# Optimization experiments

Measured on AMD Instinct MI355X. Metric: run time of the kernel, lower is better.

The kernel has to match this reference:

```python
import jax, jax.numpy as jnp
import numpy as np

B, T, C = 4, 2048, 1024
NH = 16
HS = C // NH


def setup_inputs() -> dict:
    key = jax.random.key(0)
    k1, k2, k3, k4, k5 = jax.random.split(key, 5)
    s_in = 1.0 / np.sqrt(C)
    x = jax.random.normal(k1, (B, T, C), dtype=jnp.float32)
    w_attn = jax.random.normal(k2, (C, 3 * C), dtype=jnp.float32) * s_in
    b_attn = jnp.zeros((3 * C,), dtype=jnp.float32)
    w_proj = jax.random.normal(k3, (C, C), dtype=jnp.float32) * s_in
    b_proj = jnp.zeros((C,), dtype=jnp.float32)
    return {"x": x, "w_attn": w_attn, "b_attn": b_attn,
            "w_proj": w_proj, "b_proj": b_proj}


def reference(x, w_attn, b_attn, w_proj, b_proj):
    Bsz, Tlen, Cdim = x.shape
    qkv = x @ w_attn + b_attn                      # (B,T,3C)
    q, k, v = jnp.split(qkv, 3, axis=2)
    # (B,T,C) -> (B,nh,T,hs)
    def heads(t):
        return t.reshape(Bsz, Tlen, NH, HS).transpose(0, 2, 1, 3)
    q, k, v = heads(q), heads(k), heads(v)
    scale = 1.0 / np.sqrt(HS).astype(np.float32)
    att = jnp.einsum('bhqd,bhkd->bhqk', q, k) * scale  # (B,nh,T,T)
    causal = jnp.tril(jnp.ones((Tlen, Tlen), dtype=bool))
    att = jnp.where(causal, att, -jnp.inf)
    att = jax.nn.softmax(att, axis=-1)
    y = jnp.einsum('bhqk,bhkd->bhqd', att, v)      # (B,nh,T,hs)
    y = y.transpose(0, 2, 1, 3).reshape(Bsz, Tlen, Cdim)
    return y @ w_proj + b_proj
```

## Files before the change

kernel.cpp:

```cpp
#include <hip/hip_runtime.h>
#include <hip/hip_bf16.h>

#define BB 4
#define TT 2048
#define CCH 1024
#define NHH 16
#define HSS 64
#define MROWS (BB * TT)
#define QKV_ELEMS (64 * 2048 * 64)

typedef __attribute__((ext_vector_type(8))) short short8;
typedef __attribute__((ext_vector_type(4))) float f32x4;

#define CVTPK(d, a, b) asm("v_cvt_pk_bf16_f32 %0, %1, %2" : "=v"(d) : "v"(a), "v"(b))

static __device__ __forceinline__ unsigned short bf16_of(float f) {
  union { float f; unsigned u; } v; v.f = f;
  unsigned u = v.u;
  return (unsigned short)((u + 0x7FFFu + ((u >> 16) & 1u)) >> 16);
}

__global__ __launch_bounds__(256) void cast_f32_bf16(const float* __restrict__ in,
                                                     unsigned short* __restrict__ out, int n) {
  int i = (blockIdx.x * 256 + threadIdx.x) * 4;
  if (i < n) {
    float4 f = *reinterpret_cast<const float4*>(in + i);
    ushort4 o;
    o.x = bf16_of(f.x); o.y = bf16_of(f.y); o.z = bf16_of(f.z); o.w = bf16_of(f.w);
    *reinterpret_cast<ushort4*>(out + i) = o;
  }
}

__global__ __launch_bounds__(256) void transpose_cast(const float* __restrict__ in,
                                                      unsigned short* __restrict__ out,
                                                      int K, int N) {
  __shared__ float tile[32][33];
  int k0 = blockIdx.y * 32, n0 = blockIdx.x * 32;
  int tx = threadIdx.x & 31, ty = threadIdx.x >> 5;
#pragma unroll
  for (int i = 0; i < 4; ++i)
    tile[ty + 8 * i][tx] = in[(size_t)(k0 + ty + 8 * i) * N + n0 + tx];
  __syncthreads();
#pragma unroll
  for (int i = 0; i < 4; ++i)
    out[(size_t)(n0 + ty + 8 * i) * K + k0 + tx] = bf16_of(tile[tx][ty + 8 * i]);
}

template <int MODE>
__global__ __launch_bounds__(256) void gemm_bt(const unsigned short* __restrict__ A,
                                               const unsigned short* __restrict__ Bt,
                                               const float* __restrict__ bias,
                                               float* __restrict__ outF,
                                               unsigned short* __restrict__ outQKV,
                                               int M, int N, int K) {
  __shared__ unsigned short As[2][128 * 32];
  __shared__ unsigned short Bs[2][128 * 32];
  int tid = threadIdx.x;
  int w = tid >> 6, lane = tid & 63;
  int g = lane >> 4, r16 = lane & 15;
  int wr = w >> 1, wc = w & 1;

  int nwg = (int)(gridDim.x * gridDim.y);
  int id = (int)(blockIdx.y * gridDim.x + blockIdx.x);
  int cpx = nwg >> 3;
  int swz = (id & 7) * cpx + (id >> 3);
  int m0 = (swz / (int)gridDim.x) * 128;
  int n0 = (swz % (int)gridDim.x) * 128;

  int lrow = lane >> 2;
  int lcol = (lane & 3) * 8;

#define STAGE_GEMM(buf, kt)                                                                  \
  {                                                                                          \
    _Pragma("unroll")                                                                        \
    for (int c = 0; c < 2; ++c) {                                                            \
      int rg = w * 32 + c * 16;                                                              \
      __builtin_amdgcn_global_load_lds(                                                      \
          (const __attribute__((address_space(1))) void*)(&A[(size_t)(m0 + rg + lrow) * K + (kt) + lcol]), \
          (__attribute__((address_space(3))) void*)(&As[buf][rg * 32]), 16, 0, 0);           \
      __builtin_amdgcn_global_load_lds(                                                      \
          (const __attribute__((address_space(1))) void*)(&Bt[(size_t)(n0 + rg + lrow) * K + (kt) + lcol]), \
          (__attribute__((address_space(3))) void*)(&Bs[buf][rg * 32]), 16, 0, 0);           \
    }                                                                                        \
  }

  f32x4 zero = {0.f, 0.f, 0.f, 0.f};
  f32x4 acc[4][4];
#pragma unroll
  for (int i = 0; i < 4; ++i)
#pragma unroll
    for (int n = 0; n < 4; ++n) acc[i][n] = zero;

  int nkt = K >> 5;
  STAGE_GEMM(0, 0);
  __syncthreads();
  int cur = 0;
  for (int kt = 0; kt < nkt; ++kt) {
    if (kt + 1 < nkt) STAGE_GEMM(cur ^ 1, (kt + 1) << 5);
    short8 af[4], bfr[4];
#pragma unroll
    for (int i = 0; i < 4; ++i)
      af[i] = *reinterpret_cast<const short8*>(&As[cur][(wr * 64 + i * 16 + r16) * 32 + g * 8]);
#pragma unroll
    for (int i = 0; i < 4; ++i)
      bfr[i] = *reinterpret_cast<const short8*>(&Bs[cur][(wc * 64 + i * 16 + r16) * 32 + g * 8]);
#pragma unroll
    for (int i = 0; i < 4; ++i)
#pragma unroll
      for (int n = 0; n < 4; ++n)
        acc[i][n] = __builtin_amdgcn_mfma_f32_16x16x32_bf16(af[i], bfr[n], acc[i][n], 0, 0, 0);
    __syncthreads();
    cur ^= 1;
  }
#undef STAGE_GEMM

#pragma unroll
  for (int i = 0; i < 4; ++i)
#pragma unroll
    for (int n = 0; n < 4; ++n)
#pragma unroll
      for (int j = 0; j < 4; ++j) {
        int row = m0 + wr * 64 + i * 16 + g * 4 + j;
        int col = n0 + wc * 64 + n * 16 + r16;
        float val = acc[i][n][j] + bias[col];
        if (MODE == 0) {
          outF[(size_t)row * N + col] = val;
        } else {
          int which = col >> 10, c = col & 1023;
          int h = c >> 6, d = c & 63;
          int b = row >> 11, t = row & 2047;
          if (which == 2) {
            int k5 = t & 31;
            int p = (k5 < 16) ? ((k5 >> 2) * 8 + (k5 & 3))
                              : (((k5 - 16) >> 2) * 8 + 4 + ((k5 - 16) & 3));
            int tp = (t & ~31) | p;
            outQKV[2 * (size_t)QKV_ELEMS +
                   (((size_t)(b * 16 + h) * 64 + d) * 2048 + tp)] = bf16_of(val);
          } else {
            if (which == 0) val *= 0.125f;
            outQKV[(size_t)which * QKV_ELEMS +
                   (((size_t)(b * 16 + h) * 2048 + t) * 64 + d)] = bf16_of(val);
          }
        }
      }
}

struct Frags {
  short8 kf0[2], kf1[2], vf[4];
};

static __device__ __forceinline__ void load_frags(Frags& f, int key0, int r16, int g4,
                                                  const unsigned short* __restrict__ Kp,
                                                  const unsigned short* __restrict__ Vp) {
#pragma unroll
  for (int c = 0; c < 2; ++c)
    f.kf0[c] = *reinterpret_cast<const short8*>(&Kp[(size_t)(key0 + r16) * 64 + c * 32 + g4 * 8]);
#pragma unroll
  for (int c = 0; c < 2; ++c)
    f.kf1[c] = *reinterpret_cast<const short8*>(&Kp[(size_t)(key0 + 16 + r16) * 64 + c * 32 + g4 * 8]);
#pragma unroll
  for (int dblk = 0; dblk < 4; ++dblk)
    f.vf[dblk] = *reinterpret_cast<const short8*>(
        &Vp[(size_t)(dblk * 16 + r16) * TT + key0 + g4 * 8]);
}

template <int MODE>
static __device__ __forceinline__ void compute_tile(const Frags& f, int r16, int g4,
                                                    const short8 qf[2], f32x4 o[4],
                                                    float& m, float& lsum) {
  f32x4 zero = {0.f, 0.f, 0.f, 0.f};
  f32x4 s0 = zero, s1 = zero;
  __builtin_amdgcn_s_setprio(1);
  s0 = __builtin_amdgcn_mfma_f32_16x16x32_bf16(f.kf0[0], qf[0], s0, 0, 0, 0);
  s0 = __builtin_amdgcn_mfma_f32_16x16x32_bf16(f.kf0[1], qf[1], s0, 0, 0, 0);
  if (MODE != 2) {
    s1 = __builtin_amdgcn_mfma_f32_16x16x32_bf16(f.kf1[0], qf[0], s1, 0, 0, 0);
    s1 = __builtin_amdgcn_mfma_f32_16x16x32_bf16(f.kf1[1], qf[1], s1, 0, 0, 0);
  }
  __builtin_amdgcn_s_setprio(0);

  if (MODE == 2) {
#pragma unroll
    for (int r = 0; r < 4; ++r)
      if (g4 * 4 + r > r16) s0[r] = -1e30f;
  }
  if (MODE == 1) {
#pragma unroll
    for (int r = 0; r < 4; ++r)
      if (g4 * 4 + r > r16) s1[r] = -1e30f;
  }

  float om = fmaxf(fmaxf(s0[0], s0[1]), fmaxf(s0[2], s0[3]));
  if (MODE != 2)
    om = fmaxf(om, fmaxf(fmaxf(s1[0], s1[1]), fmaxf(s1[2], s1[3])));
  om = fmaxf(om, __shfl_xor(om, 16));
  om = fmaxf(om, __shfl_xor(om, 32));
  float mn = fmaxf(m, om);
  float alpha = __expf(m - mn);
  m = mn;

  float p0[4], p1[4];
#pragma unroll
  for (int r = 0; r < 4; ++r) {
    p0[r] = __expf(s0[r] - mn);
    if (MODE != 2) p1[r] = __expf(s1[r] - mn);
  }
  float rs = (p0[0] + p0[1]) + (p0[2] + p0[3]);
  if (MODE != 2) rs += (p1[0] + p1[1]) + (p1[2] + p1[3]);
  rs += __shfl_xor(rs, 16);
  rs += __shfl_xor(rs, 32);
  lsum = lsum * alpha + rs;
#pragma unroll
  for (int dblk = 0; dblk < 4; ++dblk)
#pragma unroll
    for (int r = 0; r < 4; ++r) o[dblk][r] *= alpha;

  union { int w[4]; short8 s8; } pf;
  CVTPK(pf.w[0], p0[0], p0[1]);
  CVTPK(pf.w[1], p0[2], p0[3]);
  if (MODE != 2) {
    CVTPK(pf.w[2], p1[0], p1[1]);
    CVTPK(pf.w[3], p1[2], p1[3]);
  } else {
    pf.w[2] = 0; pf.w[3] = 0;
  }

  __builtin_amdgcn_s_setprio(1);
#pragma unroll
  for (int dblk = 0; dblk < 4; ++dblk)
    o[dblk] = __builtin_amdgcn_mfma_f32_16x16x32_bf16(f.vf[dblk], pf.s8, o[dblk], 0, 0, 0);
  __builtin_amdgcn_s_setprio(0);
}

__global__ __launch_bounds__(64, 2) void attn_kernel(const unsigned short* __restrict__ Qm,
                                                     const unsigned short* __restrict__ Km,
                                                     const unsigned short* __restrict__ Vt,
                                                     unsigned short* __restrict__ Y) {
  int lane = threadIdx.x;
  int r16 = lane & 15, g4 = lane >> 4;

  int flat = (int)(blockIdx.y * gridDim.x + blockIdx.x);
  int u = flat >> 3;
  int bh = (flat & 7) + 8 * (u & 7);
  int a = 31 - (u >> 3);
  int Q0 = a * 64;

  const unsigned short* Qp = Qm + (size_t)bh * TT * HSS;
  const unsigned short* Kp = Km + (size_t)bh * TT * HSS;
  const unsigned short* Vp = Vt + (size_t)bh * HSS * TT;

  short8 qf[4][2];
#pragma unroll
  for (int ss = 0; ss < 4; ++ss)
#pragma unroll
    for (int c = 0; c < 2; ++c)
      qf[ss][c] = *reinterpret_cast<const short8*>(
          &Qp[(size_t)(Q0 + ss * 16 + r16) * 64 + c * 32 + g4 * 8]);

  f32x4 o[4][4];
#pragma unroll
  for (int ss = 0; ss < 4; ++ss)
#pragma unroll
    for (int dblk = 0; dblk < 4; ++dblk) o[ss][dblk] = f32x4{0.f, 0.f, 0.f, 0.f};
  float m[4] = {-1e30f, -1e30f, -1e30f, -1e30f};
  float l[4] = {0.f, 0.f, 0.f, 0.f};

  Frags F;
  int nfull = a * 2;
  for (int t = 0; t < nfull; ++t) {
    load_frags(F, t << 5, r16, g4, Kp, Vp);
#pragma unroll
    for (int ss = 0; ss < 4; ++ss)
      compute_tile<0>(F, r16, g4, qf[ss], o[ss], m[ss], l[ss]);
  }
  load_frags(F, Q0, r16, g4, Kp, Vp);
  compute_tile<2>(F, r16, g4, qf[0], o[0], m[0], l[0]);
  compute_tile<1>(F, r16, g4, qf[1], o[1], m[1], l[1]);
  compute_tile<0>(F, r16, g4, qf[2], o[2], m[2], l[2]);
  compute_tile<0>(F, r16, g4, qf[3], o[3], m[3], l[3]);
  load_frags(F, Q0 + 32, r16, g4, Kp, Vp);
  compute_tile<2>(F, r16, g4, qf[2], o[2], m[2], l[2]);
  compute_tile<1>(F, r16, g4, qf[3], o[3], m[3], l[3]);

  int b = bh >> 4, h = bh & 15;
#pragma unroll
  for (int ss = 0; ss < 4; ++ss) {
    float inv = 1.0f / l[ss];
    unsigned short* yrow = Y + ((size_t)(b * TT + Q0 + ss * 16 + r16) * CCH) + h * 64;
#pragma unroll
    for (int dblk = 0; dblk < 4; ++dblk) {
      float v0 = o[ss][dblk][0] * inv, v1 = o[ss][dblk][1] * inv;
      float v2 = o[ss][dblk][2] * inv, v3 = o[ss][dblk][3] * inv;
      int wa, wb;
      CVTPK(wa, v0, v1);
      CVTPK(wb, v2, v3);
      int2 pk; pk.x = wa; pk.y = wb;
      *reinterpret_cast<int2*>(&yrow[dblk * 16 + g4 * 4]) = pk;
    }
  }
}

extern "C" void kernel_launch(void* const* d_in, const int* in_sizes, int n_in,
                              void* d_out, int out_size, void* d_ws, size_t ws_size,
                              hipStream_t stream) {
  const float* x      = (const float*)d_in[0];
  const float* w_attn = (const float*)d_in[1];
  const float* b_attn = (const float*)d_in[2];
  const float* w_proj = (const float*)d_in[3];
  const float* b_proj = (const float*)d_in[4];
  float* out = (float*)d_out;

  char* ws = (char*)d_ws;
  unsigned short* xb  = (unsigned short*)(ws + 0);
  unsigned short* wta = (unsigned short*)(ws + 16777216);
  unsigned short* wtp = (unsigned short*)(ws + 23068672);
  unsigned short* qb  = (unsigned short*)(ws + 25165824);
  unsigned short* yb  = xb;

  cast_f32_bf16<<<(MROWS * CCH) / 1024, 256, 0, stream>>>(x, xb, MROWS * CCH);
  transpose_cast<<<dim3(3 * CCH / 32, CCH / 32), 256, 0, stream>>>(w_attn, wta, CCH, 3 * CCH);
  transpose_cast<<<dim3(CCH / 32, CCH / 32), 256, 0, stream>>>(w_proj, wtp, CCH, CCH);

  {
    dim3 grid(3 * CCH / 128, MROWS / 128);
    gemm_bt<1><<<grid, 256, 0, stream>>>(xb, wta, b_attn, nullptr, qb, MROWS, 3 * CCH, CCH);
  }
  {
    dim3 grid(TT / 64, BB * NHH);
    attn_kernel<<<grid, 64, 0, stream>>>(qb, qb + (size_t)QKV_ELEMS, qb + 2 * (size_t)QKV_ELEMS, yb);
  }
  {
    dim3 grid(CCH / 128, MROWS / 128);
    gemm_bt<0><<<grid, 256, 0, stream>>>(yb, wtp, b_proj, out, nullptr, MROWS, CCH, CCH);
  }
}
```

Before: 230.0 us.

## Pair causal query blocks per workgroup and double-buffer K/V fragment loads

Each attention workgroup now processes two query blocks, a long one (31-p) and a short one (p), so every workgroup does the same amount of causal work and the grid shrinks to half as many blocks. Inside each block the K/V fragment loads are double-buffered (FA/FB), so the next tile's global loads are issued before the current tile's MFMA work and their latency can overlap with compute. The extra fragment set raises register pressure under launch_bounds(64,2), and halving the grid lowers the number of waves available to hide latency.

```diff
diff --git a/kernel.cpp b/kernel.cpp
--- a/kernel.cpp
+++ b/kernel.cpp
@@ -232,23 +232,13 @@
   __builtin_amdgcn_s_setprio(0);
 }
 
-__global__ __launch_bounds__(64, 2) void attn_kernel(const unsigned short* __restrict__ Qm,
-                                                     const unsigned short* __restrict__ Km,
-                                                     const unsigned short* __restrict__ Vt,
-                                                     unsigned short* __restrict__ Y) {
-  int lane = threadIdx.x;
-  int r16 = lane & 15, g4 = lane >> 4;
-
-  int flat = (int)(blockIdx.y * gridDim.x + blockIdx.x);
-  int u = flat >> 3;
-  int bh = (flat & 7) + 8 * (u & 7);
-  int a = 31 - (u >> 3);
+static __device__ __forceinline__ void do_qblock(int a, int r16, int g4,
+                                                 const unsigned short* __restrict__ Qp,
+                                                 const unsigned short* __restrict__ Kp,
+                                                 const unsigned short* __restrict__ Vp,
+                                                 unsigned short* __restrict__ Y,
+                                                 int b, int h) {
   int Q0 = a * 64;
-
-  const unsigned short* Qp = Qm + (size_t)bh * TT * HSS;
-  const unsigned short* Kp = Km + (size_t)bh * TT * HSS;
-  const unsigned short* Vp = Vt + (size_t)bh * HSS * TT;
-
   short8 qf[4][2];
 #pragma unroll
   for (int ss = 0; ss < 4; ++ss)
@@ -265,24 +255,37 @@
   float m[4] = {-1e30f, -1e30f, -1e30f, -1e30f};
   float l[4] = {0.f, 0.f, 0.f, 0.f};
 
-  Frags F;
+  Frags FA, FB;
   int nfull = a * 2;
-  for (int t = 0; t < nfull; ++t) {
-    load_frags(F, t << 5, r16, g4, Kp, Vp);
-#pragma unroll
-    for (int ss = 0; ss < 4; ++ss)
-      compute_tile<0>(F, r16, g4, qf[ss], o[ss], m[ss], l[ss]);
-  }
-  load_frags(F, Q0, r16, g4, Kp, Vp);
-  compute_tile<2>(F, r16, g4, qf[0], o[0], m[0], l[0]);
-  compute_tile<1>(F, r16, g4, qf[1], o[1], m[1], l[1]);
-  compute_tile<0>(F, r16, g4, qf[2], o[2], m[2], l[2]);
-  compute_tile<0>(F, r16, g4, qf[3], o[3], m[3], l[3]);
-  load_frags(F, Q0 + 32, r16, g4, Kp, Vp);
-  compute_tile<2>(F, r16, g4, qf[2], o[2], m[2], l[2]);
-  compute_tile<1>(F, r16, g4, qf[3], o[3], m[3], l[3]);
-
-  int b = bh >> 4, h = bh & 15;
+  if (nfull > 0) {
+    load_frags(FA, 0, r16, g4, Kp, Vp);
+    int t = 0;
+    while (t + 1 < nfull) {
+      load_frags(FB, (t + 1) << 5, r16, g4, Kp, Vp);
+#pragma unroll
+      for (int ss = 0; ss < 4; ++ss)
+        compute_tile<0>(FA, r16, g4, qf[ss], o[ss], m[ss], l[ss]);
+      if (t + 2 < nfull) load_frags(FA, (t + 2) << 5, r16, g4, Kp, Vp);
+#pragma unroll
+      for (int ss = 0; ss < 4; ++ss)
+        compute_tile<0>(FB, r16, g4, qf[ss], o[ss], m[ss], l[ss]);
+      t += 2;
+    }
+    if (t < nfull) {
+#pragma unroll
+      for (int ss = 0; ss < 4; ++ss)
+        compute_tile<0>(FA, r16, g4, qf[ss], o[ss], m[ss], l[ss]);
+    }
+  }
+  load_frags(FA, Q0, r16, g4, Kp, Vp);
+  load_frags(FB, Q0 + 32, r16, g4, Kp, Vp);
+  compute_tile<2>(FA, r16, g4, qf[0], o[0], m[0], l[0]);
+  compute_tile<1>(FA, r16, g4, qf[1], o[1], m[1], l[1]);
+  compute_tile<0>(FA, r16, g4, qf[2], o[2], m[2], l[2]);
+  compute_tile<0>(FA, r16, g4, qf[3], o[3], m[3], l[3]);
+  compute_tile<2>(FB, r16, g4, qf[2], o[2], m[2], l[2]);
+  compute_tile<1>(FB, r16, g4, qf[3], o[3], m[3], l[3]);
+
 #pragma unroll
   for (int ss = 0; ss < 4; ++ss) {
     float inv = 1.0f / l[ss];
@@ -300,6 +303,26 @@
   }
 }
 
+__global__ __launch_bounds__(64, 2) void attn_kernel(const unsigned short* __restrict__ Qm,
+                                                     const unsigned short* __restrict__ Km,
+                                                     const unsigned short* __restrict__ Vt,
+                                                     unsigned short* __restrict__ Y) {
+  int lane = threadIdx.x;
+  int r16 = lane & 15, g4 = lane >> 4;
+
+  int flat = (int)(blockIdx.y * gridDim.x + blockIdx.x);
+  int bh = (flat & 7) + 8 * ((flat >> 3) & 7);
+  int p = flat >> 6;
+
+  const unsigned short* Qp = Qm + (size_t)bh * TT * HSS;
+  const unsigned short* Kp = Km + (size_t)bh * TT * HSS;
+  const unsigned short* Vp = Vt + (size_t)bh * HSS * TT;
+  int b = bh >> 4, h = bh & 15;
+
+  do_qblock(31 - p, r16, g4, Qp, Kp, Vp, Y, b, h);
+  do_qblock(p, r16, g4, Qp, Kp, Vp, Y, b, h);
+}
+
 extern "C" void kernel_launch(void* const* d_in, const int* in_sizes, int n_in,
                               void* d_out, int out_size, void* d_ws, size_t ws_size,
                               hipStream_t stream) {
@@ -326,7 +349,7 @@
     gemm_bt<1><<<grid, 256, 0, stream>>>(xb, wta, b_attn, nullptr, qb, MROWS, 3 * CCH, CCH);
   }
   {
-    dim3 grid(TT / 64, BB * NHH);
+    dim3 grid(16, BB * NHH);
     attn_kernel<<<grid, 64, 0, stream>>>(qb, qb + (size_t)QKV_ELEMS, qb + 2 * (size_t)QKV_ELEMS, yb);
   }
   {
```

New measurement: 251.5 us. +9.4%, slower.
